# Kernel optimization log

Hardware: AMD Instinct MI355X
Metric: run time of the kernel (lower is better)

Reference implementation:

```python
import jax, jax.numpy as jnp
import numpy as np

DCR = 8      # depth_channel_ratio
CLIP = 0.3   # clipping_ratio
ITER = 32    # iterative_num
EPS = 1e-6


def setup_inputs() -> dict:
    key = jax.random.key(0)
    k1, k2 = jax.random.split(key)
    B, C, H, W = 8, 128, 96, 320
    input_features = jax.random.normal(k1, (B, C, H, W), dtype=jnp.float32)
    dynamic_masks = jax.random.randint(k2, (B, H, W), 0, 2, dtype=jnp.int32)
    return {"input_features": input_features, "dynamic_masks": dynamic_masks}


def _channel_selection(x):
    # Select 2*(C//DCR) channels most similar to pseudo disparity/depth ramps.
    B, C, H, W = x.shape
    disp = jnp.linspace(0.1, 1.0, H, dtype=x.dtype)                      # (H,)
    disp_full = jnp.broadcast_to(disp[None, :, None], (B, H, W)).reshape(-1)  # (B*H*W,)
    depth_full = 1.0 - disp_full
    s = jax.nn.sigmoid(x).transpose(1, 0, 2, 3).reshape(C, -1)           # (C, B*H*W)
    sn = jnp.maximum(jnp.sqrt(jnp.sum(s * s, axis=-1)), EPS)             # (C,)

    def cos_sim(v):
        vn = jnp.maximum(jnp.sqrt(jnp.sum(v * v)), EPS)
        return (s @ v) / (sn * vn)                                       # (C,)

    nsel = C // DCR
    disp_idx = jnp.argsort(-cos_sim(disp_full))[:nsel]
    depth_idx = jnp.argsort(-cos_sim(depth_full))[:nsel]
    return jnp.concatenate([disp_idx, depth_idx])                        # (2*nsel,)


def _clip_norm(v, clip_ratio):
    # per-(batch,channel) max over spatial dims, scaled, zero->1, clamp to [0,1]
    m = jnp.max(v, axis=(2, 3), keepdims=True) * clip_ratio
    m = jnp.where(m == 0, jnp.ones_like(m), m)
    return jnp.clip(v / m, 0.0, 1.0)


def reference(input_features, dynamic_masks):
    B, C, H, W = input_features.shape
    idx = _channel_selection(input_features)
    sel = input_features[:, idx]                       # (B, ns, H, W)
    # mask resolution == feature resolution, so nearest resize is identity
    m = dynamic_masks.astype(input_features.dtype)[:, None]  # (B,1,H,W) broadcast over ns
    iters = int(ITER * H / dynamic_masks.shape[1])     # == ITER here (static)

    pad_bottom = lambda t: jnp.concatenate([t, t[:, :, -1:]], axis=2)
    prop0 = pad_bottom(sel)                            # (B, ns, H+1, W)

    def step(prop, _):
        core = m * prop[:, :, 1:] + (1.0 - m) * sel    # pull values up one row where masked
        return pad_bottom(core), None

    prop, _ = jax.lax.scan(step, prop0, None, length=iters)
    prop = prop[:, :, :-1]                             # (B, ns, H, W)

    w = _clip_norm(jnp.abs(prop - sel), CLIP)
    w = jnp.max(w, axis=1, keepdims=True)              # (B,1,H,W)
    refined = w * prop + (1.0 - w) * sel
    return input_features.at[:, idx].set(refined)
```

## Files before the change

### kernel.cpp

```cpp
#include <hip/hip_runtime.h>
#include <cstdint>
#include <cstddef>

#define BB 8
#define CC 128
#define HH 96
#define WW 320
#define HW (HH*WW)
#define NSEL 32
#define NSELH 16
#define K1CH 2
#define K4CH 8

typedef float f32x4 __attribute__((ext_vector_type(4)));

__device__ __forceinline__ float sigmoidf_(float x) {
  return __builtin_amdgcn_rcpf(1.0f + __expf(-x));
}

__global__ __launch_bounds__(256) void k_copy_reduce(
    const float* __restrict__ x, float* __restrict__ out,
    double* __restrict__ partials) {
  int t = threadIdx.x;
  int chunk = blockIdx.x & (K1CH-1);
  int bc = blockIdx.x >> 1;
  const f32x4* __restrict__ xi = (const f32x4*)(x + (size_t)bc * HW);
  f32x4* __restrict__ oi = (f32x4*)(out + (size_t)bc * HW);
  float tf = 0.0f, af = 0.0f, qf = 0.0f;
  #pragma unroll 1
  for (int outer = 0; outer < 3; ++outer) {
    int base = chunk*3840 + outer*1280;
    f32x4 v[5];
    #pragma unroll
    for (int u = 0; u < 5; u++) v[u] = xi[base + u*256 + t];
    __builtin_amdgcn_sched_barrier(0);
    #pragma unroll
    for (int u = 0; u < 5; u++)
      __builtin_nontemporal_store(v[u], &oi[base + u*256 + t]);
    #pragma unroll
    for (int u = 0; u < 5; u++) {
      int j = base + u*256 + t;
      int h = j / (WW/4);
      float d = 0.1f + (float)h * (0.9f/95.0f);
      float s0 = sigmoidf_(v[u].x), s1 = sigmoidf_(v[u].y);
      float s2 = sigmoidf_(v[u].z), s3 = sigmoidf_(v[u].w);
      float ts = (s0+s1)+(s2+s3);
      tf += ts;
      af += ts * d;
      qf += (s0*s0+s1*s1)+(s2*s2+s3*s3);
    }
  }
  __shared__ double sh[3][256];
  sh[0][t]=(double)tf; sh[1][t]=(double)af; sh[2][t]=(double)qf;
  __syncthreads();
  for (int ofs=128; ofs>0; ofs>>=1) {
    if (t < ofs) {
      sh[0][t]+=sh[0][t+ofs];
      sh[1][t]+=sh[1][t+ofs];
      sh[2][t]+=sh[2][t+ofs];
    }
    __syncthreads();
  }
  if (t==0) {
    int p = bc*K1CH + chunk;
    partials[p*3+0]=sh[0][0];
    partials[p*3+1]=sh[1][0];
    partials[p*3+2]=sh[2][0];
  }
}

__global__ __launch_bounds__(CC) void k_select(
    const double* __restrict__ partials, int* __restrict__ idx) {
  int c = threadIdx.x;
  double T=0.0, A=0.0, Q=0.0;
  for (int b=0;b<BB;b++) {
    for (int ch=0; ch<K1CH; ch++) {
      int p = (b*CC + c)*K1CH + ch;
      T += partials[p*3+0];
      A += partials[p*3+1];
      Q += partials[p*3+2];
    }
  }
  double sn = sqrt(Q); if (sn < 1e-6) sn = 1e-6;
  double c1 = A / sn;
  double c2 = (T - A) / sn;
  __shared__ double s1[CC], s2[CC];
  s1[c]=c1; s2[c]=c2;
  __syncthreads();
  int r1=0, r2=0;
  for (int j=0;j<CC;j++) {
    r1 += (s1[j] > c1) || (s1[j]==c1 && j<c);
    r2 += (s2[j] > c2) || (s2[j]==c2 && j<c);
  }
  if (r1 < NSELH) idx[r1] = c;
  if (r2 < NSELH) idx[NSELH + r2] = c;
}

__global__ __launch_bounds__(64) void k_runs(
    const int* __restrict__ mask, uint8_t* __restrict__ kk) {
  int b = blockIdx.x / 5;
  int w = (blockIdx.x % 5)*64 + threadIdx.x;
  const int* __restrict__ mcol = mask + (size_t)b*HW + w;
  unsigned long long lo=0ull, hi=0ull;
  #pragma unroll
  for (int h=0; h<64; ++h) lo |= (unsigned long long)(mcol[h*WW]!=0) << h;
  #pragma unroll
  for (int h=64; h<95; ++h) hi |= (unsigned long long)(mcol[h*WW]!=0) << (h-64);
  uint8_t* __restrict__ kcol = kk + (size_t)b*HW + w;
  #pragma unroll
  for (int h=0; h<96; ++h) {
    unsigned long long s;
    if (h == 0)      s = lo;
    else if (h < 64) s = (lo >> h) | (hi << (64-h));
    else             s = hi >> (h-64);
    int run = __builtin_ctzll(~s | (1ull<<33));
    kcol[h*WW] = (uint8_t)(run > 32 ? 32 : run);
  }
}

__global__ __launch_bounds__(256) void k_maxdiff(
    const float* __restrict__ x, const int* __restrict__ idx,
    const uint8_t* __restrict__ kk, float* __restrict__ pmax) {
  int chunk = blockIdx.x & (K4CH-1);
  int bc32 = blockIdx.x >> 3;
  int b = bc32 >> 5;
  int c = bc32 & 31;
  int ic = idx[c];
  const float* __restrict__ base = x + ((size_t)b*CC + ic)*HW;
  const uint8_t* __restrict__ kb = kk + (size_t)b*HW;
  float mx = 0.0f;
  int lo = chunk * (HW/4/K4CH), hiend = lo + (HW/4/K4CH);
  for (int j = lo + threadIdx.x; j < hiend; j += 256) {
    f32x4 sel = ((const f32x4*)base)[j];
    uchar4 kv  = ((const uchar4*)kb)[j];
    int h = j / (WW/4);
    int w4 = (j - h*(WW/4))*4;
    float p0 = base[(h+(int)kv.x)*WW + w4+0];
    float p1 = base[(h+(int)kv.y)*WW + w4+1];
    float p2 = base[(h+(int)kv.z)*WW + w4+2];
    float p3 = base[(h+(int)kv.w)*WW + w4+3];
    mx = fmaxf(mx, fmaxf(fmaxf(fabsf(p0-sel.x), fabsf(p1-sel.y)),
                         fmaxf(fabsf(p2-sel.z), fabsf(p3-sel.w))));
  }
  __shared__ float sh[256];
  sh[threadIdx.x]=mx; __syncthreads();
  for (int ofs=128; ofs>0; ofs>>=1) {
    if ((int)threadIdx.x<ofs) sh[threadIdx.x]=fmaxf(sh[threadIdx.x], sh[threadIdx.x+ofs]);
    __syncthreads();
  }
  if (threadIdx.x==0) pmax[blockIdx.x] = sh[0];
}

__global__ __launch_bounds__(WW) void k_refine(
    const float* __restrict__ x, const int* __restrict__ idx,
    const uint8_t* __restrict__ kk, const float* __restrict__ pmax,
    float* __restrict__ out) {
  int bh = blockIdx.x;
  int b = bh / HH, h = bh - b*HH;
  int w = threadIdx.x;
  __shared__ int sidx[NSEL];
  __shared__ float smc[NSEL];
  if (threadIdx.x < NSEL) {
    int c = threadIdx.x;
    sidx[c] = idx[c];
    float m = 0.0f;
    #pragma unroll
    for (int ch=0; ch<K4CH; ch++) m = fmaxf(m, pmax[(b*NSEL + c)*K4CH + ch]);
    m *= 0.3f;
    if (m == 0.0f) m = 1.0f;
    smc[c] = m;
  }
  __syncthreads();
  int r = h + (int)kk[(size_t)bh*WW + w];
  float sel[NSEL], prop[NSEL];
  float wmax = 0.0f;
  #pragma unroll
  for (int c=0;c<NSEL;c++) {
    const float* __restrict__ base = x + ((size_t)b*CC + sidx[c])*HW;
    sel[c]  = base[h*WW + w];
    prop[c] = base[r*WW + w];
    float v = fabsf(prop[c]-sel[c]) / smc[c];
    wmax = fmaxf(wmax, fminf(v, 1.0f));
  }
  #pragma unroll
  for (int c=0;c<NSEL;c++) {
    float rf = wmax*prop[c] + (1.0f - wmax)*sel[c];
    __builtin_nontemporal_store(rf, &out[((size_t)b*CC + sidx[c])*HW + h*WW + w]);
  }
}

extern "C" void kernel_launch(void* const* d_in, const int* in_sizes, int n_in,
                              void* d_out, int out_size, void* d_ws, size_t ws_size,
                              hipStream_t stream) {
  const float* x   = (const float*)d_in[0];
  const int* mask  = (const int*)d_in[1];
  float* out       = (float*)d_out;

  char* ws = (char*)d_ws;
  double* partials = (double*)(ws);
  int*    idx      = (int*)(ws + 49152);
  float*  pmax     = (float*)(ws + 49152 + 128);
  uint8_t* kk      = (uint8_t*)(ws + 49152 + 128 + 8192);

  k_copy_reduce<<<BB*CC*K1CH, 256, 0, stream>>>(x, out, partials);
  k_select<<<1, CC, 0, stream>>>(partials, idx);
  k_runs<<<BB*5, 64, 0, stream>>>(mask, kk);
  k_maxdiff<<<BB*NSEL*K4CH, 256, 0, stream>>>(x, idx, kk, pmax);
  k_refine<<<BB*HH, WW, 0, stream>>>(x, idx, kk, pmax, out);
}
```

Measured before the change: 101.0 us.

## Split copy from reduction and skip copying channels that get refined

Separates the full-tensor copy from the sigmoid reduction pass. After channel selection, a new kernel copies only the unselected channels, using a per-channel flag written by the selection kernel. This removes redundant writes for the selected channels, which refine overwrites anyway. The cost is a second full read of the input for the copy, plus one more kernel launch.

```diff
diff --git a/kernel.cpp b/kernel.cpp
--- a/kernel.cpp
+++ b/kernel.cpp
@@ -18,14 +18,12 @@
   return __builtin_amdgcn_rcpf(1.0f + __expf(-x));
 }
 
-__global__ __launch_bounds__(256) void k_copy_reduce(
-    const float* __restrict__ x, float* __restrict__ out,
-    double* __restrict__ partials) {
+__global__ __launch_bounds__(256) void k_reduce(
+    const float* __restrict__ x, double* __restrict__ partials) {
   int t = threadIdx.x;
   int chunk = blockIdx.x & (K1CH-1);
   int bc = blockIdx.x >> 1;
   const f32x4* __restrict__ xi = (const f32x4*)(x + (size_t)bc * HW);
-  f32x4* __restrict__ oi = (f32x4*)(out + (size_t)bc * HW);
   float tf = 0.0f, af = 0.0f, qf = 0.0f;
   #pragma unroll 1
   for (int outer = 0; outer < 3; ++outer) {
@@ -33,10 +31,6 @@
     f32x4 v[5];
     #pragma unroll
     for (int u = 0; u < 5; u++) v[u] = xi[base + u*256 + t];
-    __builtin_amdgcn_sched_barrier(0);
-    #pragma unroll
-    for (int u = 0; u < 5; u++)
-      __builtin_nontemporal_store(v[u], &oi[base + u*256 + t]);
     #pragma unroll
     for (int u = 0; u < 5; u++) {
       int j = base + u*256 + t;
@@ -70,7 +64,8 @@
 }
 
 __global__ __launch_bounds__(CC) void k_select(
-    const double* __restrict__ partials, int* __restrict__ idx) {
+    const double* __restrict__ partials, int* __restrict__ idx,
+    int* __restrict__ selflag) {
   int c = threadIdx.x;
   double T=0.0, A=0.0, Q=0.0;
   for (int b=0;b<BB;b++) {
@@ -92,6 +87,7 @@
     r1 += (s1[j] > c1) || (s1[j]==c1 && j<c);
     r2 += (s2[j] > c2) || (s2[j]==c2 && j<c);
   }
+  selflag[c] = (r1 < NSELH || r2 < NSELH) ? 1 : 0;
   if (r1 < NSELH) idx[r1] = c;
   if (r2 < NSELH) idx[NSELH + r2] = c;
 }
@@ -151,6 +147,27 @@
   if (threadIdx.x==0) pmax[blockIdx.x] = sh[0];
 }
 
+__global__ __launch_bounds__(256) void k_copy_unsel(
+    const float* __restrict__ x, const int* __restrict__ selflag,
+    float* __restrict__ out) {
+  int chunk = blockIdx.x & (K1CH-1);
+  int bc = blockIdx.x >> 1;
+  if (selflag[bc & (CC-1)]) return;
+  int t = threadIdx.x;
+  const f32x4* __restrict__ xi = (const f32x4*)(x + (size_t)bc * HW);
+  f32x4* __restrict__ oi = (f32x4*)(out + (size_t)bc * HW);
+  #pragma unroll 1
+  for (int outer = 0; outer < 3; ++outer) {
+    int base = chunk*3840 + outer*1280;
+    f32x4 v[5];
+    #pragma unroll
+    for (int u = 0; u < 5; u++) v[u] = xi[base + u*256 + t];
+    #pragma unroll
+    for (int u = 0; u < 5; u++)
+      __builtin_nontemporal_store(v[u], &oi[base + u*256 + t]);
+  }
+}
+
 __global__ __launch_bounds__(WW) void k_refine(
     const float* __restrict__ x, const int* __restrict__ idx,
     const uint8_t* __restrict__ kk, const float* __restrict__ pmax,
@@ -199,11 +216,13 @@
   char* ws = (char*)d_ws;
   double* partials = (double*)(ws);
   int*    idx      = (int*)(ws + 49152);
-  float*  pmax     = (float*)(ws + 49152 + 128);
-  uint8_t* kk      = (uint8_t*)(ws + 49152 + 128 + 8192);
-
-  k_copy_reduce<<<BB*CC*K1CH, 256, 0, stream>>>(x, out, partials);
-  k_select<<<1, CC, 0, stream>>>(partials, idx);
+  int*    selflag  = (int*)(ws + 49152 + 128);
+  float*  pmax     = (float*)(ws + 49152 + 128 + 512);
+  uint8_t* kk      = (uint8_t*)(ws + 49152 + 128 + 512 + 8192);
+
+  k_reduce<<<BB*CC*K1CH, 256, 0, stream>>>(x, partials);
+  k_select<<<1, CC, 0, stream>>>(partials, idx, selflag);
+  k_copy_unsel<<<BB*CC*K1CH, 256, 0, stream>>>(x, selflag, out);
   k_runs<<<BB*5, 64, 0, stream>>>(mask, kk);
   k_maxdiff<<<BB*NSEL*K4CH, 256, 0, stream>>>(x, idx, kk, pmax);
   k_refine<<<BB*HH, WW, 0, stream>>>(x, idx, kk, pmax, out);
```

New measurement: 111.9 us. 1.11x slower.
